# Optimization experiments

Measured on AMD Instinct MI355X. Metric: run time of the kernel, lower is better.

## Reference

```python
import math
import jax, jax.numpy as jnp
import numpy as np

B, L, H, E = 2, 2048, 8, 64
S, D = 2048, 64


def _row_mask(index, sub_len, win_len, log_l):
    # Faithful to torch code, including the swapped-arg call convention:
    # called with sub_len = L (query len), win_len = S (key len).
    mask = np.zeros(win_len, dtype=np.float32)
    if (win_len // sub_len) * 2 * log_l > index:
        mask[: index + 1] = 1.0
    else:
        while index >= 0:
            if index - log_l + 1 < 0:
                mask[:index] = 1.0
                break
            mask[index - log_l + 1 : index + 1] = 1.0
            for i in range(log_l):
                new_index = index - log_l + 1 - 2 ** i
                if index - new_index <= sub_len and new_index >= 0:
                    mask[new_index] = 1.0
            index -= sub_len
    return mask


def _log_mask(win_len, sub_len):
    # mirrors LogSparseAttention.log_mask(L, S) with its swapped row_mask call
    log_l = math.ceil(np.log2(win_len))  # log2 of query length L
    m = np.zeros((win_len, sub_len), dtype=np.float32)
    for i in range(win_len):
        m[i] = _row_mask(i, win_len, sub_len, log_l)
    return jnp.asarray(m)[None, None]  # [1,1,L,S]


_MASK = _log_mask(L, S)


def setup_inputs() -> dict:
    key = jax.random.key(0)
    kq, kk, kv = jax.random.split(key, 3)
    return {
        "queries": jax.random.normal(kq, (B, L, H, E), dtype=jnp.float32),
        "keys": jax.random.normal(kk, (B, S, H, E), dtype=jnp.float32),
        "values": jax.random.normal(kv, (B, S, H, D), dtype=jnp.float32),
        "attention_mask": jnp.ones((1,), dtype=bool),  # unused, as in the torch module
    }


def reference(queries, keys, values, attention_mask):
    scale = 1.0 / math.sqrt(queries.shape[-1])
    scores = jnp.einsum("blhe,bshe->bhls", queries, keys)  # [B,H,L,S]
    mask = _MASK[:, :, : scores.shape[-2], : scores.shape[-1]]
    scores = scores * mask + (-1e9) * (1.0 - mask)
    A = jax.nn.softmax(scale * scores, axis=-1)  # dropout = identity in eval
    V = jnp.einsum("bhls,bshd->blhd", A, values)  # [B,L,H,D]
    return V
```

## Files before the change

kernel.cpp:

```cpp
#include <hip/hip_runtime.h>


#define BB 2
#define LL 2048
#define HH 8
#define EE 64
#define SS 2048

template<int CTRL>
__device__ __forceinline__ float dpp_add(float v) {
    int t = __builtin_amdgcn_mov_dpp(__float_as_int(v), CTRL, 0xF, 0xF, false);
    return v + __int_as_float(t);
}

__global__ __launch_bounds__(256) void logsparse_attn_kernel(
    const float* __restrict__ Q,
    const float* __restrict__ K,
    const float* __restrict__ V,
    float* __restrict__ O)
{
    const int lane = threadIdx.x & 63;
    const int wv   = threadIdx.x >> 6;
    const int lb  = ((blockIdx.x & 7) << 10) | (blockIdx.x >> 3);
    const int row = lb * 4 + wv;
    const int l  = row % LL;
    const int bh = row / LL;
    const int h  = bh & (HH - 1);
    const int b  = bh / HH;

    const int t = lane & 15;
    const int g = lane >> 4;

    const size_t qbase = (((size_t)b * LL + l) * HH + h) * (size_t)EE;
    const float4 qf = *(const float4*)(Q + qbase + 4 * t);

    const size_t bhoff = (size_t)b * ((size_t)SS * HH * EE) + (size_t)h * EE;
    const float* Kb = K + bhoff;
    const float* Vb = V + bhoff;

    int ntaps, nkeys, w0;
    if (l < 22) { ntaps = 0; nkeys = l + 1; w0 = 0; }
    else {
        w0 = l - 10;
        ntaps = 32 - __clz(w0);
        if (ntaps > 11) ntaps = 11;
        nkeys = ntaps + 11;
    }

    float  sc[6];
    float4 vv[6];
    #pragma unroll
    for (int c = 0; c < 6; ++c) {
        const int n  = 4 * c + g;
        const int nc = (n < nkeys) ? n : (nkeys - 1);
        int key;
        if (l < 22)           key = nc;
        else if (nc < ntaps)  key = w0 - (1 << (ntaps - 1 - nc));
        else                  key = w0 + (nc - ntaps);
        const size_t off = ((size_t)key << 9) + 4 * t;
        const float4 kf = *(const float4*)(Kb + off);
        vv[c] = *(const float4*)(Vb + off);

        float p = qf.x * kf.x + qf.y * kf.y + qf.z * kf.z + qf.w * kf.w;
        p = dpp_add<0xB1>(p);
        p = dpp_add<0x4E>(p);
        p = dpp_add<0x124>(p);
        p = dpp_add<0x128>(p);
        sc[c] = (n < nkeys) ? p * 0.125f : -1e30f;
    }

    float mg = sc[0];
    #pragma unroll
    for (int c = 1; c < 6; ++c) mg = fmaxf(mg, sc[c]);

    float  lsum = 0.0f;
    float4 acc  = {0.f, 0.f, 0.f, 0.f};
    #pragma unroll
    for (int c = 0; c < 6; ++c) {
        const float w = __expf(sc[c] - mg);
        lsum  += w;
        acc.x += w * vv[c].x;
        acc.y += w * vv[c].y;
        acc.z += w * vv[c].z;
        acc.w += w * vv[c].w;
    }

    float M = mg;
    M = fmaxf(M, __shfl_xor(M, 16, 64));
    M = fmaxf(M, __shfl_xor(M, 32, 64));
    const float r = __expf(mg - M);
    lsum  *= r;
    acc.x *= r; acc.y *= r; acc.z *= r; acc.w *= r;

    lsum  += __shfl_xor(lsum, 16, 64);    lsum  += __shfl_xor(lsum, 32, 64);
    acc.x += __shfl_xor(acc.x, 16, 64);   acc.x += __shfl_xor(acc.x, 32, 64);
    acc.y += __shfl_xor(acc.y, 16, 64);   acc.y += __shfl_xor(acc.y, 32, 64);
    acc.z += __shfl_xor(acc.z, 16, 64);   acc.z += __shfl_xor(acc.z, 32, 64);
    acc.w += __shfl_xor(acc.w, 16, 64);   acc.w += __shfl_xor(acc.w, 32, 64);

    if (g == 0) {
        const float inv = 1.0f / lsum;
        float4 o;
        o.x = acc.x * inv; o.y = acc.y * inv;
        o.z = acc.z * inv; o.w = acc.w * inv;
        *(float4*)(O + qbase + 4 * t) = o;
    }
}

extern "C" void kernel_launch(void* const* d_in, const int* in_sizes, int n_in,
                              void* d_out, int out_size, void* d_ws, size_t ws_size,
                              hipStream_t stream) {
    const float* Q = (const float*)d_in[0];
    const float* K = (const float*)d_in[1];
    const float* V = (const float*)d_in[2];
    float* O = (float*)d_out;

    const int rows   = BB * HH * LL;
    const int blocks = rows / 4;
    hipLaunchKernelGGL(logsparse_attn_kernel, dim3(blocks), dim3(256), 0, stream,
                       Q, K, V, O);
}
```

Measured before the change: 91.24 us.

## Pre-pack K and V into interleaved bf16 workspace before sparse attention

A new pre-pass kernel converts K and V to bf16 with round-to-nearest-even and interleaves them per (b,h,s) into a 256-byte record. The attention kernel then fetches each key's K and V with a single 16-byte load per lane, so gathered traffic is halved and spread over fewer cache lines. The cost is an extra kernel launch that reads all of K and V and writes the workspace, plus bf16 rounding error in the keys and values.

After: 94.44 us. +3.5%, slower.

```diff
diff --git a/kernel.cpp b/kernel.cpp
--- a/kernel.cpp
+++ b/kernel.cpp
@@ -7,16 +7,60 @@
 #define EE 64
 #define SS 2048
 
+__device__ __forceinline__ unsigned short bf16_rne(float f) {
+    unsigned int u = __float_as_uint(f);
+    unsigned int r = u + 0x7FFFu + ((u >> 16) & 1u);
+    return (unsigned short)(r >> 16);
+}
+
 template<int CTRL>
 __device__ __forceinline__ float dpp_add(float v) {
     int t = __builtin_amdgcn_mov_dpp(__float_as_int(v), CTRL, 0xF, 0xF, false);
     return v + __int_as_float(t);
 }
 
+__device__ __forceinline__ void unpack8(const uint4 kv, float* e) {
+    e[0] = __int_as_float((int)(kv.x << 16));
+    e[1] = __int_as_float((int)(kv.x & 0xFFFF0000u));
+    e[2] = __int_as_float((int)(kv.y << 16));
+    e[3] = __int_as_float((int)(kv.y & 0xFFFF0000u));
+    e[4] = __int_as_float((int)(kv.z << 16));
+    e[5] = __int_as_float((int)(kv.z & 0xFFFF0000u));
+    e[6] = __int_as_float((int)(kv.w << 16));
+    e[7] = __int_as_float((int)(kv.w & 0xFFFF0000u));
+}
+
+__global__ __launch_bounds__(256) void pack_kv_kernel(
+    const float* __restrict__ K, const float* __restrict__ V,
+    unsigned short* __restrict__ P)
+{
+    const int j = blockIdx.x * 256 + threadIdx.x;
+    const int p = j & 7;
+    const int h = (j >> 3) & (HH - 1);
+    const int s = (j >> 6) & (SS - 1);
+    const int b = j >> 17;
+    const size_t src = (((size_t)b * SS + s) * HH + h) * EE + 8 * p;
+    const float4 k0 = *(const float4*)(K + src);
+    const float4 k1 = *(const float4*)(K + src + 4);
+    const float4 v0 = *(const float4*)(V + src);
+    const float4 v1 = *(const float4*)(V + src + 4);
+    uint4 kw, vw;
+    kw.x = bf16_rne(k0.x) | ((unsigned)bf16_rne(k0.y) << 16);
+    kw.y = bf16_rne(k0.z) | ((unsigned)bf16_rne(k0.w) << 16);
+    kw.z = bf16_rne(k1.x) | ((unsigned)bf16_rne(k1.y) << 16);
+    kw.w = bf16_rne(k1.z) | ((unsigned)bf16_rne(k1.w) << 16);
+    vw.x = bf16_rne(v0.x) | ((unsigned)bf16_rne(v0.y) << 16);
+    vw.y = bf16_rne(v0.z) | ((unsigned)bf16_rne(v0.w) << 16);
+    vw.z = bf16_rne(v1.x) | ((unsigned)bf16_rne(v1.y) << 16);
+    vw.w = bf16_rne(v1.z) | ((unsigned)bf16_rne(v1.w) << 16);
+    const size_t n = ((size_t)b * HH + h) * SS + s;
+    *(uint4*)(P + n * 128 + 8 * p)      = kw;
+    *(uint4*)(P + n * 128 + 64 + 8 * p) = vw;
+}
+
 __global__ __launch_bounds__(256) void logsparse_attn_kernel(
     const float* __restrict__ Q,
-    const float* __restrict__ K,
-    const float* __restrict__ V,
+    const unsigned short* __restrict__ P,
     float* __restrict__ O)
 {
     const int lane = threadIdx.x & 63;
@@ -25,18 +69,21 @@
     const int row = lb * 4 + wv;
     const int l  = row % LL;
     const int bh = row / LL;
-    const int h  = bh & (HH - 1);
-    const int b  = bh / HH;
 
-    const int t = lane & 15;
-    const int g = lane >> 4;
+    const int t  = lane & 15;
+    const int g  = lane >> 4;
+    const int t8 = t & 7;
 
-    const size_t qbase = (((size_t)b * LL + l) * HH + h) * (size_t)EE;
-    const float4 qf = *(const float4*)(Q + qbase + 4 * t);
+    const size_t qbase = ((size_t)(bh / HH) * LL + l) * HH * EE + (size_t)(bh & (HH - 1)) * EE;
+    float qr[8];
+    {
+        const float4 a  = *(const float4*)(Q + qbase + 8 * t8);
+        const float4 b4 = *(const float4*)(Q + qbase + 8 * t8 + 4);
+        qr[0] = a.x;  qr[1] = a.y;  qr[2] = a.z;  qr[3] = a.w;
+        qr[4] = b4.x; qr[5] = b4.y; qr[6] = b4.z; qr[7] = b4.w;
+    }
 
-    const size_t bhoff = (size_t)b * ((size_t)SS * HH * EE) + (size_t)h * EE;
-    const float* Kb = K + bhoff;
-    const float* Vb = V + bhoff;
+    const unsigned short* Pbh = P + (size_t)bh * SS * 128;
 
     int ntaps, nkeys, w0;
     if (l < 22) { ntaps = 0; nkeys = l + 1; w0 = 0; }
@@ -47,8 +94,7 @@
         nkeys = ntaps + 11;
     }
 
-    float  sc[6];
-    float4 vv[6];
+    uint4 kv[6];
     #pragma unroll
     for (int c = 0; c < 6; ++c) {
         const int n  = 4 * c + g;
@@ -57,53 +103,63 @@
         if (l < 22)           key = nc;
         else if (nc < ntaps)  key = w0 - (1 << (ntaps - 1 - nc));
         else                  key = w0 + (nc - ntaps);
-        const size_t off = ((size_t)key << 9) + 4 * t;
-        const float4 kf = *(const float4*)(Kb + off);
-        vv[c] = *(const float4*)(Vb + off);
+        kv[c] = *(const uint4*)(Pbh + ((size_t)key << 7) + 8 * t);
+    }
 
-        float p = qf.x * kf.x + qf.y * kf.y + qf.z * kf.z + qf.w * kf.w;
+    float sc[6];
+    #pragma unroll
+    for (int c = 0; c < 6; ++c) {
+        float e[8];
+        unpack8(kv[c], e);
+        float p = qr[0]*e[0] + qr[1]*e[1] + qr[2]*e[2] + qr[3]*e[3]
+                + qr[4]*e[4] + qr[5]*e[5] + qr[6]*e[6] + qr[7]*e[7];
+        p = (t < 8) ? p : 0.0f;
         p = dpp_add<0xB1>(p);
         p = dpp_add<0x4E>(p);
         p = dpp_add<0x124>(p);
         p = dpp_add<0x128>(p);
-        sc[c] = (n < nkeys) ? p * 0.125f : -1e30f;
+        sc[c] = ((4 * c + g) < nkeys) ? p * 0.125f : -1e30f;
     }
 
     float mg = sc[0];
     #pragma unroll
     for (int c = 1; c < 6; ++c) mg = fmaxf(mg, sc[c]);
 
-    float  lsum = 0.0f;
-    float4 acc  = {0.f, 0.f, 0.f, 0.f};
+    float lsum = 0.0f;
+    float acc[8] = {0.f,0.f,0.f,0.f,0.f,0.f,0.f,0.f};
     #pragma unroll
     for (int c = 0; c < 6; ++c) {
         const float w = __expf(sc[c] - mg);
-        lsum  += w;
-        acc.x += w * vv[c].x;
-        acc.y += w * vv[c].y;
-        acc.z += w * vv[c].z;
-        acc.w += w * vv[c].w;
+        lsum += w;
+        float e[8];
+        unpack8(kv[c], e);
+        #pragma unroll
+        for (int j = 0; j < 8; ++j) acc[j] += w * e[j];
     }
 
     float M = mg;
     M = fmaxf(M, __shfl_xor(M, 16, 64));
     M = fmaxf(M, __shfl_xor(M, 32, 64));
     const float r = __expf(mg - M);
-    lsum  *= r;
-    acc.x *= r; acc.y *= r; acc.z *= r; acc.w *= r;
+    lsum *= r;
+    #pragma unroll
+    for (int j = 0; j < 8; ++j) acc[j] *= r;
 
-    lsum  += __shfl_xor(lsum, 16, 64);    lsum  += __shfl_xor(lsum, 32, 64);
-    acc.x += __shfl_xor(acc.x, 16, 64);   acc.x += __shfl_xor(acc.x, 32, 64);
-    acc.y += __shfl_xor(acc.y, 16, 64);   acc.y += __shfl_xor(acc.y, 32, 64);
-    acc.z += __shfl_xor(acc.z, 16, 64);   acc.z += __shfl_xor(acc.z, 32, 64);
-    acc.w += __shfl_xor(acc.w, 16, 64);   acc.w += __shfl_xor(acc.w, 32, 64);
+    lsum += __shfl_xor(lsum, 16, 64);
+    lsum += __shfl_xor(lsum, 32, 64);
+    #pragma unroll
+    for (int j = 0; j < 8; ++j) {
+        acc[j] += __shfl_xor(acc[j], 16, 64);
+        acc[j] += __shfl_xor(acc[j], 32, 64);
+    }
 
-    if (g == 0) {
+    if (g == 0 && t >= 8) {
         const float inv = 1.0f / lsum;
-        float4 o;
-        o.x = acc.x * inv; o.y = acc.y * inv;
-        o.z = acc.z * inv; o.w = acc.w * inv;
-        *(float4*)(O + qbase + 4 * t) = o;
+        float4 o0, o1;
+        o0.x = acc[0]*inv; o0.y = acc[1]*inv; o0.z = acc[2]*inv; o0.w = acc[3]*inv;
+        o1.x = acc[4]*inv; o1.y = acc[5]*inv; o1.z = acc[6]*inv; o1.w = acc[7]*inv;
+        *(float4*)(O + qbase + 8 * t8)     = o0;
+        *(float4*)(O + qbase + 8 * t8 + 4) = o1;
     }
 }
 
@@ -114,9 +170,10 @@
     const float* K = (const float*)d_in[1];
     const float* V = (const float*)d_in[2];
     float* O = (float*)d_out;
+    unsigned short* P = (unsigned short*)d_ws;
 
-    const int rows   = BB * HH * LL;
-    const int blocks = rows / 4;
-    hipLaunchKernelGGL(logsparse_attn_kernel, dim3(blocks), dim3(256), 0, stream,
-                       Q, K, V, O);
+    hipLaunchKernelGGL(pack_kv_kernel, dim3((BB*SS*HH*8)/256), dim3(256), 0, stream,
+                       K, V, P);
+    hipLaunchKernelGGL(logsparse_attn_kernel, dim3((BB*HH*LL)/4), dim3(256), 0, stream,
+                       Q, P, O);
 }
```

## Prefetch per-XCD K/V slices into L2 and use nontemporal Q/O accesses

Applied to the files above, without the earlier changes.

Each block first loads a strided slice of the K and V rows belonging to the (b,h) pairs mapped to its XCD, folding the values into a dummy sink so the compiler keeps the loads. This warms each XCD's L2 with the data its sparse gathers will touch, in place of scattered cold misses. Q loads and O stores become nontemporal so they do not evict the K/V lines. The cost is an extra full pass over K and V plus a dependency that serialises the prefetch ahead of the softmax reduction.

Result: slower. 95.97 us (+5.2%).

```diff
diff --git a/kernel.cpp b/kernel.cpp
--- a/kernel.cpp
+++ b/kernel.cpp
@@ -6,6 +6,8 @@
 #define HH 8
 #define EE 64
 #define SS 2048
+
+typedef float floatx4 __attribute__((ext_vector_type(4)));
 
 template<int CTRL>
 __device__ __forceinline__ float dpp_add(float v) {
@@ -21,18 +23,39 @@
 {
     const int lane = threadIdx.x & 63;
     const int wv   = threadIdx.x >> 6;
-    const int lb  = ((blockIdx.x & 7) << 10) | (blockIdx.x >> 3);
+    const int xcd = blockIdx.x & 7;
+    const int q   = blockIdx.x >> 3;
+    const int lb  = (xcd << 10) | q;
     const int row = lb * 4 + wv;
     const int l  = row % LL;
     const int bh = row / LL;
     const int h  = bh & (HH - 1);
     const int b  = bh / HH;
 
+    float sink = 0.0f;
+    {
+        const int p = q * 256 + (int)threadIdx.x;
+        if (p < 131072) {
+            const int tensor = p >> 16;
+            const int r    = p & 65535;
+            const int pair = r >> 15;
+            const int u    = r & 32767;
+            const int s    = u >> 4;
+            const int part = u & 15;
+            const int pbh  = xcd * 2 + pair;
+            const size_t off = ((size_t)(pbh >> 3) * SS + s) * 512
+                             + (size_t)(pbh & 7) * 64 + part * 4;
+            const float4 pv = tensor ? *(const float4*)(V + off)
+                                     : *(const float4*)(K + off);
+            sink = pv.x + pv.y + pv.z + pv.w;
+        }
+    }
+
     const int t = lane & 15;
     const int g = lane >> 4;
 
     const size_t qbase = (((size_t)b * LL + l) * HH + h) * (size_t)EE;
-    const float4 qf = *(const float4*)(Q + qbase + 4 * t);
+    const floatx4 qf = __builtin_nontemporal_load((const floatx4*)(Q + qbase + 4 * t));
 
     const size_t bhoff = (size_t)b * ((size_t)SS * HH * EE) + (size_t)h * EE;
     const float* Kb = K + bhoff;
@@ -84,6 +107,7 @@
         acc.z += w * vv[c].z;
         acc.w += w * vv[c].w;
     }
+    lsum += sink * 0.0f;
 
     float M = mg;
     M = fmaxf(M, __shfl_xor(M, 16, 64));
@@ -100,10 +124,10 @@
 
     if (g == 0) {
         const float inv = 1.0f / lsum;
-        float4 o;
+        floatx4 o;
         o.x = acc.x * inv; o.y = acc.y * inv;
         o.z = acc.z * inv; o.w = acc.w * inv;
-        *(float4*)(O + qbase + 4 * t) = o;
+        __builtin_nontemporal_store(o, (floatx4*)(O + qbase + 4 * t));
     }
 }
 
```
